# Kernel optimization log

Measured on AMD Instinct MI355X. Metric: run time of the kernel, lower is better.

The kernel has to match this reference:

```python
import jax, jax.numpy as jnp
import numpy as np

IN_FEATS = 768   # xlm-roberta-base hidden size
HIDDEN = 128     # hardcoded in GCNEncoder
OUT_FEATS = 128
NUM_GRAPHS = 1024
NODES_PER_GRAPH = 256
N = NUM_GRAPHS * NODES_PER_GRAPH
N_CLASS = 2


def setup_inputs() -> dict:
    key = jax.random.key(0)
    ks = jax.random.split(key, 12)
    s = lambda fan_in: 1.0 / np.sqrt(fan_in)
    return {
        "x": jax.random.normal(ks[0], (N, IN_FEATS), dtype=jnp.float32),
        "prompt_node": jax.random.normal(ks[1], (IN_FEATS,), dtype=jnp.float32),
        "class_nodes": jax.random.normal(ks[2], (N_CLASS, IN_FEATS), dtype=jnp.float32),
        "W1": jax.random.uniform(ks[3], (IN_FEATS, HIDDEN), jnp.float32, -s(IN_FEATS), s(IN_FEATS)),
        "b1": jnp.zeros((HIDDEN,), jnp.float32),
        "W2": jax.random.uniform(ks[4], (HIDDEN, OUT_FEATS), jnp.float32, -s(HIDDEN), s(HIDDEN)),
        "b2": jnp.zeros((OUT_FEATS,), jnp.float32),
        "Wfc": jax.random.uniform(ks[5], (OUT_FEATS, N_CLASS), jnp.float32, -s(OUT_FEATS), s(OUT_FEATS)),
        "bfc": jnp.zeros((N_CLASS,), jnp.float32),
        "num_graphs": NUM_GRAPHS,
    }


def _gcn_conv(h_in, W, b, src, dst, num_nodes):
    # PyG GCNConv: add self loops, symmetric norm D^-1/2 (A+I) D^-1/2, then X W + b.
    deg = jax.ops.segment_sum(jnp.ones_like(src, dtype=h_in.dtype), dst,
                              num_segments=num_nodes) + 1.0  # +1 for self loop
    dinv = deg ** -0.5
    h = h_in @ W                                    # [num_nodes, out]
    norm = dinv[src] * dinv[dst]                    # [E]
    agg = jax.ops.segment_sum(h[src] * norm[:, None], dst, num_segments=num_nodes)
    agg = agg + (dinv * dinv)[:, None] * h          # self-loop contribution
    return agg + b


def reference(x, prompt_node, class_nodes, W1, b1, W2, b2, Wfc, bfc, num_graphs):
    G = int(num_graphs)
    N_orig = x.shape[0]
    n_per = N_orig // G
    n_cls = class_nodes.shape[0]
    total = N_orig + G + G * n_cls

    # construct_prompted_graph: append prompt nodes then class nodes (tiled per graph)
    full_x = jnp.concatenate([
        x,
        jnp.broadcast_to(prompt_node, (G, prompt_node.shape[0])),
        jnp.tile(class_nodes, (G, 1)),
    ], axis=0)

    # star edges: node -> prompt, prompt -> class; then to_undirected (both dirs)
    src1 = jnp.arange(N_orig)
    dst1 = N_orig + jnp.repeat(jnp.arange(G), n_per)
    src2 = jnp.repeat(N_orig + jnp.arange(G), n_cls)
    dst2 = N_orig + G + jnp.arange(G * n_cls)
    src = jnp.concatenate([src1, src2, dst1, dst2])
    dst = jnp.concatenate([dst1, dst2, src1, src2])

    h = _gcn_conv(full_x, W1, b1, src, dst, total)
    h = jax.nn.relu(h)  # dropout omitted (eval mode)
    h = _gcn_conv(h, W2, b2, src, dst, total)

    class_idx = N_orig + G + jnp.arange(G * n_cls)
    class_emb = h[class_idx]                         # [G*n_cls, OUT_FEATS]
    logits = class_emb @ Wfc + bfc                   # [G*n_cls, 2]
    return jax.nn.log_softmax(logits, axis=-1)
```

## Files before the change

### kernel.cpp

```cpp
#include <hip/hip_runtime.h>
#include <math.h>

namespace {
constexpr int IN_FEATS = 768;
constexpr int HIDDEN   = 128;
constexpr int G        = 1024;
constexpr int NPG      = 256;
constexpr int C4       = IN_FEATS / 4;
constexpr int NT       = 384;
}

__global__ __launch_bounds__(NT, 6) void fused_kernel(
    const float* __restrict__ x, const float* __restrict__ prompt,
    const float* __restrict__ cls,
    const float* __restrict__ W1, const float* __restrict__ b1,
    const float* __restrict__ W2, const float* __restrict__ b2,
    const float* __restrict__ Wfc, const float* __restrict__ bfc,
    float* __restrict__ out)
{
    __shared__ float   S[IN_FEATS];
    __shared__ float   pc[3 * IN_FEATS];
    __shared__ float4  partA[2][C4];
    __shared__ float4  pb[3][HIDDEN];
    __shared__ float   rbuf[3][HIDDEN];
    __shared__ float   red[2][2];

    const int g   = blockIdx.x;
    const int tid = threadIdx.x;
    const float ainv = 1.0f / sqrtf(518.0f);

    for (int i = tid; i < 3 * IN_FEATS; i += NT)
        pc[i] = (i < IN_FEATS) ? prompt[i] : cls[i - IN_FEATS];

    const int p  = tid / C4;
    const int c4 = tid % C4;
    const float4* xp = reinterpret_cast<const float4*>(x) +
                       ((size_t)g * NPG + p) * C4 + c4;
    float4 a0 = make_float4(0.f, 0.f, 0.f, 0.f);
    float4 a1 = a0, a2 = a0, a3 = a0;
    for (int i = 0; i < NPG / 2; i += 4) {
        const float4 v0 = xp[(size_t)(2 * (i + 0)) * C4];
        const float4 v1 = xp[(size_t)(2 * (i + 1)) * C4];
        const float4 v2 = xp[(size_t)(2 * (i + 2)) * C4];
        const float4 v3 = xp[(size_t)(2 * (i + 3)) * C4];
        a0.x += v0.x; a0.y += v0.y; a0.z += v0.z; a0.w += v0.w;
        a1.x += v1.x; a1.y += v1.y; a1.z += v1.z; a1.w += v1.w;
        a2.x += v2.x; a2.y += v2.y; a2.z += v2.z; a2.w += v2.w;
        a3.x += v3.x; a3.y += v3.y; a3.z += v3.z; a3.w += v3.w;
    }
    float4 s;
    s.x = (a0.x + a1.x) + (a2.x + a3.x);
    s.y = (a0.y + a1.y) + (a2.y + a3.y);
    s.z = (a0.z + a1.z) + (a2.z + a3.z);
    s.w = (a0.w + a1.w) + (a2.w + a3.w);
    partA[p][c4] = s;
    __syncthreads();
    if (tid < C4) {
        const float4 q0 = partA[0][tid], q1 = partA[1][tid];
        reinterpret_cast<float4*>(S)[tid] =
            make_float4(q0.x + q1.x, q0.y + q1.y, q0.z + q1.z, q0.w + q1.w);
    }
    __syncthreads();

    {
        const int seg = tid >> 7;
        const int j   = tid & (HIDDEN - 1);
        const int cb  = seg * 256;
        const float* w1p = W1 + (size_t)cb * HIDDEN + j;
        float t = 0.f, hp = 0.f, h0 = 0.f, h1 = 0.f;
        #pragma unroll 4
        for (int cc = 0; cc < 256; ++cc) {
            const float w = w1p[(size_t)cc * HIDDEN];
            const int  c = cb + cc;
            t  = fmaf(S[c], w, t);
            hp = fmaf(pc[c], w, hp);
            h0 = fmaf(pc[IN_FEATS + c], w, h0);
            h1 = fmaf(pc[2 * IN_FEATS + c], w, h1);
        }
        pb[seg][j] = make_float4(t, hp, h0, h1);
    }
    __syncthreads();
    if (tid < HIDDEN) {
        const float4 q0 = pb[0][tid], q1 = pb[1][tid], q2 = pb[2][tid];
        const float t  = (q0.x + q1.x) + q2.x;
        const float hp = (q0.y + q1.y) + q2.y;
        const float h0 = (q0.z + q1.z) + q2.z;
        const float h1 = (q0.w + q1.w) + q2.w;
        const float b  = b1[tid];
        const float C1 = ainv * (h0 + h1) + hp * (1.0f / 259.0f) + b;
        rbuf[0][tid] = fmaxf(fmaf(ainv, t, C1), 0.f);
        rbuf[1][tid] = fmaxf(fmaf(ainv, hp, fmaf(0.5f, h0, b)), 0.f);
        rbuf[2][tid] = fmaxf(fmaf(ainv, hp, fmaf(0.5f, h1, b)), 0.f);
    }
    __syncthreads();

    float u = 0.f, u0 = 0.f, u1 = 0.f;
    if (tid < HIDDEN) {
        const float* w2p = W2 + tid;
        #pragma unroll 4
        for (int c = 0; c < HIDDEN; ++c) {
            const float w = w2p[(size_t)c * HIDDEN];
            u  = fmaf(rbuf[0][c], w, u);
            u0 = fmaf(rbuf[1][c], w, u0);
            u1 = fmaf(rbuf[2][c], w, u1);
        }
    }

    const float bfc0 = bfc[0], bfc1 = bfc[1];
    for (int k = 0; k < 2; ++k) {
        float p0 = 0.f, p1 = 0.f;
        if (tid < HIDDEN) {
            const float uk = (k == 0) ? u0 : u1;
            const float v  = fmaf(ainv, u, fmaf(0.5f, uk, b2[tid]));
            p0 = v * Wfc[tid * 2 + 0];
            p1 = v * Wfc[tid * 2 + 1];
            #pragma unroll
            for (int off = 32; off > 0; off >>= 1) {
                p0 += __shfl_down(p0, off);
                p1 += __shfl_down(p1, off);
            }
            if ((tid & 63) == 0) { red[tid >> 6][0] = p0; red[tid >> 6][1] = p1; }
        }
        __syncthreads();
        if (tid == 0) {
            const float l0 = red[0][0] + red[1][0] + bfc0;
            const float l1 = red[0][1] + red[1][1] + bfc1;
            const float m   = fmaxf(l0, l1);
            const float lse = m + logf(expf(l0 - m) + expf(l1 - m));
            float* o = out + ((size_t)g * 2 + k) * 2;
            o[0] = l0 - lse;
            o[1] = l1 - lse;
        }
        __syncthreads();
    }
}

extern "C" void kernel_launch(void* const* d_in, const int* in_sizes, int n_in,
                              void* d_out, int out_size, void* d_ws, size_t ws_size,
                              hipStream_t stream) {
    const float* x      = (const float*)d_in[0];
    const float* prompt = (const float*)d_in[1];
    const float* cls    = (const float*)d_in[2];
    const float* W1     = (const float*)d_in[3];
    const float* b1     = (const float*)d_in[4];
    const float* W2     = (const float*)d_in[5];
    const float* b2     = (const float*)d_in[6];
    const float* Wfc    = (const float*)d_in[7];
    const float* bfc    = (const float*)d_in[8];
    float* out = (float*)d_out;

    fused_kernel<<<G, NT, 0, stream>>>(x, prompt, cls, W1, b1, W2, b2,
                                       Wfc, bfc, out);
}
```

Measured before the change: 167.0 us.

## Process two graphs per block to amortize W1/W2 loads and prompt/class work

Each block now handles two graphs, so the W1 and W2 matrices, the prompt and the class-node projections are read and computed once per pair of graphs instead of once per graph. The x reads use nontemporal loads, and the prompt/class vectors are read straight from global memory instead of being staged in shared memory. The cost is half as many blocks (512 on a large GPU), a lower occupancy hint, and more serialized reductions per block, which may leave the memory-bound x stream less parallel.

```diff
diff --git a/kernel.cpp b/kernel.cpp
--- a/kernel.cpp
+++ b/kernel.cpp
@@ -8,9 +8,12 @@
 constexpr int NPG      = 256;
 constexpr int C4       = IN_FEATS / 4;
 constexpr int NT       = 384;
+constexpr int GPB      = 2;
+constexpr int NB       = G / GPB;
+typedef float f32x4 __attribute__((ext_vector_type(4)));
 }
 
-__global__ __launch_bounds__(NT, 6) void fused_kernel(
+__global__ __launch_bounds__(NT, 3) void fused_kernel(
     const float* __restrict__ x, const float* __restrict__ prompt,
     const float* __restrict__ cls,
     const float* __restrict__ W1, const float* __restrict__ b1,
@@ -18,120 +21,136 @@
     const float* __restrict__ Wfc, const float* __restrict__ bfc,
     float* __restrict__ out)
 {
-    __shared__ float   S[IN_FEATS];
-    __shared__ float   pc[3 * IN_FEATS];
-    __shared__ float4  partA[2][C4];
-    __shared__ float4  pb[3][HIDDEN];
-    __shared__ float   rbuf[3][HIDDEN];
-    __shared__ float   red[2][2];
+    __shared__ __align__(16) float S[GPB][IN_FEATS];
+    __shared__ f32x4  partA[2][C4];
+    __shared__ float  pb[3][5][HIDDEN];
+    __shared__ __align__(16) float rbuf[4][HIDDEN];
+    __shared__ float  red[2][2];
 
-    const int g   = blockIdx.x;
+    const int g0  = blockIdx.x * GPB;
     const int tid = threadIdx.x;
     const float ainv = 1.0f / sqrtf(518.0f);
 
-    for (int i = tid; i < 3 * IN_FEATS; i += NT)
-        pc[i] = (i < IN_FEATS) ? prompt[i] : cls[i - IN_FEATS];
-
     const int p  = tid / C4;
     const int c4 = tid % C4;
-    const float4* xp = reinterpret_cast<const float4*>(x) +
-                       ((size_t)g * NPG + p) * C4 + c4;
-    float4 a0 = make_float4(0.f, 0.f, 0.f, 0.f);
-    float4 a1 = a0, a2 = a0, a3 = a0;
-    for (int i = 0; i < NPG / 2; i += 4) {
-        const float4 v0 = xp[(size_t)(2 * (i + 0)) * C4];
-        const float4 v1 = xp[(size_t)(2 * (i + 1)) * C4];
-        const float4 v2 = xp[(size_t)(2 * (i + 2)) * C4];
-        const float4 v3 = xp[(size_t)(2 * (i + 3)) * C4];
-        a0.x += v0.x; a0.y += v0.y; a0.z += v0.z; a0.w += v0.w;
-        a1.x += v1.x; a1.y += v1.y; a1.z += v1.z; a1.w += v1.w;
-        a2.x += v2.x; a2.y += v2.y; a2.z += v2.z; a2.w += v2.w;
-        a3.x += v3.x; a3.y += v3.y; a3.z += v3.z; a3.w += v3.w;
+    const f32x4* xb = reinterpret_cast<const f32x4*>(x);
+    for (int gg = 0; gg < GPB; ++gg) {
+        const f32x4* xp = xb + ((size_t)(g0 + gg) * NPG + p) * C4 + c4;
+        f32x4 a0 = (f32x4)0.0f;
+        f32x4 a1 = a0, a2 = a0, a3 = a0;
+        for (int i = 0; i < NPG / 2; i += 4) {
+            const f32x4 v0 = __builtin_nontemporal_load(xp + (size_t)(2 * (i + 0)) * C4);
+            const f32x4 v1 = __builtin_nontemporal_load(xp + (size_t)(2 * (i + 1)) * C4);
+            const f32x4 v2 = __builtin_nontemporal_load(xp + (size_t)(2 * (i + 2)) * C4);
+            const f32x4 v3 = __builtin_nontemporal_load(xp + (size_t)(2 * (i + 3)) * C4);
+            a0 += v0; a1 += v1; a2 += v2; a3 += v3;
+        }
+        partA[p][c4] = (a0 + a1) + (a2 + a3);
+        __syncthreads();
+        if (tid < C4) {
+            const f32x4 q0 = partA[0][tid], q1 = partA[1][tid];
+            *reinterpret_cast<f32x4*>(&S[gg][tid * 4]) = q0 + q1;
+        }
+        __syncthreads();
     }
-    float4 s;
-    s.x = (a0.x + a1.x) + (a2.x + a3.x);
-    s.y = (a0.y + a1.y) + (a2.y + a3.y);
-    s.z = (a0.z + a1.z) + (a2.z + a3.z);
-    s.w = (a0.w + a1.w) + (a2.w + a3.w);
-    partA[p][c4] = s;
-    __syncthreads();
-    if (tid < C4) {
-        const float4 q0 = partA[0][tid], q1 = partA[1][tid];
-        reinterpret_cast<float4*>(S)[tid] =
-            make_float4(q0.x + q1.x, q0.y + q1.y, q0.z + q1.z, q0.w + q1.w);
-    }
-    __syncthreads();
 
     {
         const int seg = tid >> 7;
         const int j   = tid & (HIDDEN - 1);
         const int cb  = seg * 256;
         const float* w1p = W1 + (size_t)cb * HIDDEN + j;
-        float t = 0.f, hp = 0.f, h0 = 0.f, h1 = 0.f;
-        #pragma unroll 4
-        for (int cc = 0; cc < 256; ++cc) {
-            const float w = w1p[(size_t)cc * HIDDEN];
-            const int  c = cb + cc;
-            t  = fmaf(S[c], w, t);
-            hp = fmaf(pc[c], w, hp);
-            h0 = fmaf(pc[IN_FEATS + c], w, h0);
-            h1 = fmaf(pc[2 * IN_FEATS + c], w, h1);
+        float t0 = 0.f, t1 = 0.f, hp = 0.f, h0 = 0.f, h1 = 0.f;
+        for (int cc = 0; cc < 256; cc += 4) {
+            const int c = cb + cc;
+            const f32x4 s0 = *reinterpret_cast<const f32x4*>(&S[0][c]);
+            const f32x4 s1 = *reinterpret_cast<const f32x4*>(&S[1][c]);
+            const f32x4 pv = *reinterpret_cast<const f32x4*>(prompt + c);
+            const f32x4 k0 = *reinterpret_cast<const f32x4*>(cls + c);
+            const f32x4 k1 = *reinterpret_cast<const f32x4*>(cls + IN_FEATS + c);
+            const float w0 = w1p[(size_t)(cc + 0) * HIDDEN];
+            const float w1 = w1p[(size_t)(cc + 1) * HIDDEN];
+            const float w2 = w1p[(size_t)(cc + 2) * HIDDEN];
+            const float w3 = w1p[(size_t)(cc + 3) * HIDDEN];
+            t0 = fmaf(s0.x, w0, t0); t1 = fmaf(s1.x, w0, t1);
+            hp = fmaf(pv.x, w0, hp); h0 = fmaf(k0.x, w0, h0); h1 = fmaf(k1.x, w0, h1);
+            t0 = fmaf(s0.y, w1, t0); t1 = fmaf(s1.y, w1, t1);
+            hp = fmaf(pv.y, w1, hp); h0 = fmaf(k0.y, w1, h0); h1 = fmaf(k1.y, w1, h1);
+            t0 = fmaf(s0.z, w2, t0); t1 = fmaf(s1.z, w2, t1);
+            hp = fmaf(pv.z, w2, hp); h0 = fmaf(k0.z, w2, h0); h1 = fmaf(k1.z, w2, h1);
+            t0 = fmaf(s0.w, w3, t0); t1 = fmaf(s1.w, w3, t1);
+            hp = fmaf(pv.w, w3, hp); h0 = fmaf(k0.w, w3, h0); h1 = fmaf(k1.w, w3, h1);
         }
-        pb[seg][j] = make_float4(t, hp, h0, h1);
+        pb[seg][0][j] = t0; pb[seg][1][j] = t1;
+        pb[seg][2][j] = hp; pb[seg][3][j] = h0; pb[seg][4][j] = h1;
     }
     __syncthreads();
     if (tid < HIDDEN) {
-        const float4 q0 = pb[0][tid], q1 = pb[1][tid], q2 = pb[2][tid];
-        const float t  = (q0.x + q1.x) + q2.x;
-        const float hp = (q0.y + q1.y) + q2.y;
-        const float h0 = (q0.z + q1.z) + q2.z;
-        const float h1 = (q0.w + q1.w) + q2.w;
+        const float t0 = pb[0][0][tid] + pb[1][0][tid] + pb[2][0][tid];
+        const float t1 = pb[0][1][tid] + pb[1][1][tid] + pb[2][1][tid];
+        const float hp = pb[0][2][tid] + pb[1][2][tid] + pb[2][2][tid];
+        const float h0 = pb[0][3][tid] + pb[1][3][tid] + pb[2][3][tid];
+        const float h1 = pb[0][4][tid] + pb[1][4][tid] + pb[2][4][tid];
         const float b  = b1[tid];
         const float C1 = ainv * (h0 + h1) + hp * (1.0f / 259.0f) + b;
-        rbuf[0][tid] = fmaxf(fmaf(ainv, t, C1), 0.f);
-        rbuf[1][tid] = fmaxf(fmaf(ainv, hp, fmaf(0.5f, h0, b)), 0.f);
-        rbuf[2][tid] = fmaxf(fmaf(ainv, hp, fmaf(0.5f, h1, b)), 0.f);
+        rbuf[0][tid] = fmaxf(fmaf(ainv, t0, C1), 0.f);
+        rbuf[1][tid] = fmaxf(fmaf(ainv, t1, C1), 0.f);
+        rbuf[2][tid] = fmaxf(fmaf(ainv, hp, fmaf(0.5f, h0, b)), 0.f);
+        rbuf[3][tid] = fmaxf(fmaf(ainv, hp, fmaf(0.5f, h1, b)), 0.f);
     }
     __syncthreads();
 
-    float u = 0.f, u0 = 0.f, u1 = 0.f;
+    float u0 = 0.f, u1 = 0.f, uc0 = 0.f, uc1 = 0.f;
     if (tid < HIDDEN) {
         const float* w2p = W2 + tid;
-        #pragma unroll 4
-        for (int c = 0; c < HIDDEN; ++c) {
-            const float w = w2p[(size_t)c * HIDDEN];
-            u  = fmaf(rbuf[0][c], w, u);
-            u0 = fmaf(rbuf[1][c], w, u0);
-            u1 = fmaf(rbuf[2][c], w, u1);
+        for (int c = 0; c < HIDDEN; c += 4) {
+            const f32x4 r0 = *reinterpret_cast<const f32x4*>(&rbuf[0][c]);
+            const f32x4 r1 = *reinterpret_cast<const f32x4*>(&rbuf[1][c]);
+            const f32x4 q0 = *reinterpret_cast<const f32x4*>(&rbuf[2][c]);
+            const f32x4 q1 = *reinterpret_cast<const f32x4*>(&rbuf[3][c]);
+            const float wa = w2p[(size_t)(c + 0) * HIDDEN];
+            const float wb = w2p[(size_t)(c + 1) * HIDDEN];
+            const float wc = w2p[(size_t)(c + 2) * HIDDEN];
+            const float wd = w2p[(size_t)(c + 3) * HIDDEN];
+            u0  = fmaf(r0.x, wa, u0);  u1  = fmaf(r1.x, wa, u1);
+            uc0 = fmaf(q0.x, wa, uc0); uc1 = fmaf(q1.x, wa, uc1);
+            u0  = fmaf(r0.y, wb, u0);  u1  = fmaf(r1.y, wb, u1);
+            uc0 = fmaf(q0.y, wb, uc0); uc1 = fmaf(q1.y, wb, uc1);
+            u0  = fmaf(r0.z, wc, u0);  u1  = fmaf(r1.z, wc, u1);
+            uc0 = fmaf(q0.z, wc, uc0); uc1 = fmaf(q1.z, wc, uc1);
+            u0  = fmaf(r0.w, wd, u0);  u1  = fmaf(r1.w, wd, u1);
+            uc0 = fmaf(q0.w, wd, uc0); uc1 = fmaf(q1.w, wd, uc1);
         }
     }
 
     const float bfc0 = bfc[0], bfc1 = bfc[1];
-    for (int k = 0; k < 2; ++k) {
-        float p0 = 0.f, p1 = 0.f;
-        if (tid < HIDDEN) {
-            const float uk = (k == 0) ? u0 : u1;
-            const float v  = fmaf(ainv, u, fmaf(0.5f, uk, b2[tid]));
-            p0 = v * Wfc[tid * 2 + 0];
-            p1 = v * Wfc[tid * 2 + 1];
-            #pragma unroll
-            for (int off = 32; off > 0; off >>= 1) {
-                p0 += __shfl_down(p0, off);
-                p1 += __shfl_down(p1, off);
+    for (int gg = 0; gg < GPB; ++gg) {
+        for (int k = 0; k < 2; ++k) {
+            float p0 = 0.f, p1 = 0.f;
+            if (tid < HIDDEN) {
+                const float ug = (gg == 0) ? u0 : u1;
+                const float uk = (k == 0) ? uc0 : uc1;
+                const float v  = fmaf(ainv, ug, fmaf(0.5f, uk, b2[tid]));
+                p0 = v * Wfc[tid * 2 + 0];
+                p1 = v * Wfc[tid * 2 + 1];
+                #pragma unroll
+                for (int off = 32; off > 0; off >>= 1) {
+                    p0 += __shfl_down(p0, off);
+                    p1 += __shfl_down(p1, off);
+                }
+                if ((tid & 63) == 0) { red[tid >> 6][0] = p0; red[tid >> 6][1] = p1; }
             }
-            if ((tid & 63) == 0) { red[tid >> 6][0] = p0; red[tid >> 6][1] = p1; }
+            __syncthreads();
+            if (tid == 0) {
+                const float l0 = red[0][0] + red[1][0] + bfc0;
+                const float l1 = red[0][1] + red[1][1] + bfc1;
+                const float m   = fmaxf(l0, l1);
+                const float lse = m + logf(expf(l0 - m) + expf(l1 - m));
+                float* o = out + ((size_t)(g0 + gg) * 2 + k) * 2;
+                o[0] = l0 - lse;
+                o[1] = l1 - lse;
+            }
+            __syncthreads();
         }
-        __syncthreads();
-        if (tid == 0) {
-            const float l0 = red[0][0] + red[1][0] + bfc0;
-            const float l1 = red[0][1] + red[1][1] + bfc1;
-            const float m   = fmaxf(l0, l1);
-            const float lse = m + logf(expf(l0 - m) + expf(l1 - m));
-            float* o = out + ((size_t)g * 2 + k) * 2;
-            o[0] = l0 - lse;
-            o[1] = l1 - lse;
-        }
-        __syncthreads();
     }
 }
 
@@ -149,6 +168,6 @@
     const float* bfc    = (const float*)d_in[8];
     float* out = (float*)d_out;
 
-    fused_kernel<<<G, NT, 0, stream>>>(x, prompt, cls, W1, b1, W2, b2,
-                                       Wfc, bfc, out);
+    fused_kernel<<<NB, NT, 0, stream>>>(x, prompt, cls, W1, b1, W2, b2,
+                                        Wfc, bfc, out);
 }
```

New measurement: 145.5 us. -12.9%, faster.
